# Kernel optimization log

Measured on AMD Instinct MI355X. Metric: run time of the kernel, lower is better.

Reference implementation:

```python
import jax, jax.numpy as jnp
import numpy as np

GAMMA = 0.7


def setup_inputs() -> dict:
    key = jax.random.key(0)
    k1, k2, k3 = jax.random.split(key, 3)
    K, N, M = 8, 2_000_000, 50_000
    states_x = jax.random.normal(k1, (K, N, 3), dtype=jnp.float32)
    x_target = jax.random.normal(k2, (N, 3), dtype=jnp.float32)
    molecule_id = jnp.sort(jax.random.randint(k3, (N,), 0, M, dtype=jnp.int64))
    return {
        "states_x": states_x,
        "x_target": x_target,
        "molecule_id": molecule_id,
        "num_molecules": M,
    }


def reference(states_x, x_target, molecule_id, num_molecules):
    # states_x: (K, N, 3) = refinement states 1..K (state 0 is already dropped)
    # x_target: (N, 3); molecule_id: (N,) segment ids
    K = states_x.shape[0]
    dtype = x_target.dtype
    # exponential weights gamma^(K-1-k), normalized
    w = jnp.power(jnp.asarray(GAMMA, dtype), (K - 1) - jnp.arange(K, dtype=dtype))
    w = w / w.sum()
    # per-atom squared distance per state: (K, N)
    sq = ((states_x - x_target[None]) ** 2).sum(axis=-1)
    # segment-reduce over molecules: sums (M, K), counts (M,)
    sums = jax.ops.segment_sum(sq.T, molecule_id, num_segments=num_molecules)
    counts = jax.ops.segment_sum(
        jnp.ones((molecule_id.shape[0],), dtype=dtype), molecule_id,
        num_segments=num_molecules)
    valid = counts > 0  # pt.unique only iterates over ids that appear
    means = sums / jnp.maximum(counts, 1)[:, None]  # (M, K) per-molecule mean sq dist
    per_state = (means * valid[:, None].astype(dtype)).sum(axis=0) / valid.sum().astype(dtype)
    return (w * per_state).sum()
```

## Files before the change

kernel.cpp:

```cpp
#include <hip/hip_runtime.h>

#define GAMMA 0.7f
static constexpr int K = 8;
static constexpr int P = 1024;


__global__ void __launch_bounds__(256)
main_fused(const float* __restrict__ sx,
           const float* __restrict__ xt,
           const int* __restrict__ mol,
           float* __restrict__ partials,
           int* __restrict__ bcounts,
           int N) {
    const int tid = threadIdx.x;
    const int b0  = blockIdx.x * P;
    const int n0  = b0 + tid * 4;

    __shared__ int ids[P + 2];
    int* w = ids + 1;

    int myid[4];
    if (n0 + 3 < N) {
        int4 v = *reinterpret_cast<const int4*>(mol + n0);
        myid[0] = v.x; myid[1] = v.y; myid[2] = v.z; myid[3] = v.w;
    } else {
#pragma unroll
        for (int j = 0; j < 4; ++j) {
            int n = n0 + j;
            myid[j] = (n < N) ? mol[n] : 0x7fffffff;
        }
    }
#pragma unroll
    for (int j = 0; j < 4; ++j) w[tid * 4 + j] = myid[j];
    if (tid == 0)   ids[0]     = (b0 == 0) ? -1 : mol[b0 - 1];
    if (tid == 255) ids[P + 1] = (b0 + P >= N) ? 0x7fffffff : mol[b0 + P];
    __syncthreads();

    float inv[4];
    int nb = 0;
#pragma unroll
    for (int j = 0; j < 4; ++j) {
        const int p  = tid * 4 + j;
        const int id = myid[j];
        const bool valid = (b0 + p < N);
        const int prevv = (j > 0) ? myid[j - 1] : ids[p];
        if (valid && prevv != id) ++nb;
        if (!valid) { inv[j] = 0.0f; continue; }
        if (j > 0 && myid[j - 1] == id) { inv[j] = inv[j - 1]; continue; }

        int lo = 0, hi = p;
        while (lo < hi) { int m = (lo + hi) >> 1; if (w[m] < id) lo = m + 1; else hi = m; }
        const int s = lo;
        lo = p + 1; hi = P;
        while (lo < hi) { int m = (lo + hi) >> 1; if (w[m] <= id) lo = m + 1; else hi = m; }
        const int e = lo;

        int gstart = b0 + s;
        if (s == 0 && ids[0] == id) {
            lo = 0; hi = b0;
            while (lo < hi) { int m = (lo + hi) >> 1; if (mol[m] < id) lo = m + 1; else hi = m; }
            gstart = lo;
        }
        int gend = b0 + e;
        if (e == P && ids[P + 1] == id) {
            lo = b0 + P; hi = N;
            while (lo < hi) { int m = (lo + hi) >> 1; if (mol[m] <= id) lo = m + 1; else hi = m; }
            gend = lo;
        }
        inv[j] = 1.0f / (float)(gend - gstart);
    }

    float acc[K];
#pragma unroll
    for (int k = 0; k < K; ++k) acc[k] = 0.0f;

    if (n0 + 3 < N) {
        const float4* tp = reinterpret_cast<const float4*>(xt + (size_t)n0 * 3);
        float4 t0 = tp[0], t1 = tp[1], t2 = tp[2];
        float tg[12] = {t0.x, t0.y, t0.z, t0.w, t1.x, t1.y,
                        t1.z, t1.w, t2.x, t2.y, t2.z, t2.w};
#pragma unroll
        for (int k = 0; k < K; ++k) {
            const float4* sp = reinterpret_cast<const float4*>(
                sx + (size_t)k * N * 3 + (size_t)n0 * 3);
            float4 s0 = sp[0], s1 = sp[1], s2 = sp[2];
            float sv[12] = {s0.x, s0.y, s0.z, s0.w, s1.x, s1.y,
                            s1.z, s1.w, s2.x, s2.y, s2.z, s2.w};
#pragma unroll
            for (int j = 0; j < 4; ++j) {
                float dx = sv[3 * j + 0] - tg[3 * j + 0];
                float dy = sv[3 * j + 1] - tg[3 * j + 1];
                float dz = sv[3 * j + 2] - tg[3 * j + 2];
                acc[k] += (dx * dx + dy * dy + dz * dz) * inv[j];
            }
        }
    } else if (n0 < N) {
        for (int n = n0; n < N; ++n) {
            const int j = n - n0;
            float tx = xt[(size_t)n * 3 + 0];
            float ty = xt[(size_t)n * 3 + 1];
            float tz = xt[(size_t)n * 3 + 2];
#pragma unroll
            for (int k = 0; k < K; ++k) {
                const float* s = sx + (size_t)k * N * 3 + (size_t)n * 3;
                float dx = s[0] - tx, dy = s[1] - ty, dz = s[2] - tz;
                acc[k] += (dx * dx + dy * dy + dz * dz) * inv[j];
            }
        }
    }

#pragma unroll
    for (int k = 0; k < K; ++k)
#pragma unroll
        for (int off = 32; off > 0; off >>= 1)
            acc[k] += __shfl_down(acc[k], off, 64);
#pragma unroll
    for (int off = 32; off > 0; off >>= 1) nb += __shfl_down(nb, off, 64);

    __shared__ float lds[4][K];
    __shared__ int   bl[4];
    const int wave = tid >> 6, lane = tid & 63;
    if (lane == 0) {
        bl[wave] = nb;
#pragma unroll
        for (int k = 0; k < K; ++k) lds[wave][k] = acc[k];
    }
    __syncthreads();
    if (tid < K) {
        int k = tid;
        partials[(size_t)blockIdx.x * K + k] =
            lds[0][k] + lds[1][k] + lds[2][k] + lds[3][k];
    }
    if (tid == 0)
        bcounts[blockIdx.x] = bl[0] + bl[1] + bl[2] + bl[3];
}

__global__ void __launch_bounds__(256)
final_kernel(const float* __restrict__ partials,
             const int* __restrict__ bcounts, int nblocks,
             float* __restrict__ out) {
    const int t = threadIdx.x;

    int vc = 0;
    for (int i = t; i < nblocks; i += 256) vc += bcounts[i];
#pragma unroll
    for (int off = 32; off > 0; off >>= 1) vc += __shfl_down(vc, off, 64);

    float acc[K];
#pragma unroll
    for (int k = 0; k < K; ++k) acc[k] = 0.0f;
    for (int i = t; i < nblocks; i += 256) {
#pragma unroll
        for (int k = 0; k < K; ++k) acc[k] += partials[(size_t)i * K + k];
    }
#pragma unroll
    for (int k = 0; k < K; ++k)
#pragma unroll
        for (int off = 32; off > 0; off >>= 1)
            acc[k] += __shfl_down(acc[k], off, 64);

    __shared__ int vlds[4];
    __shared__ float plds[4][K];
    const int wave = t >> 6, lane = t & 63;
    if (lane == 0) {
        vlds[wave] = vc;
#pragma unroll
        for (int k = 0; k < K; ++k) plds[wave][k] = acc[k];
    }
    __syncthreads();

    if (t == 0) {
        int V = vlds[0] + vlds[1] + vlds[2] + vlds[3];
        float w[K], wsum = 0.0f, g = 1.0f;
        for (int j = 0; j < K; ++j) {
            w[K - 1 - j] = g;
            wsum += g;
            g *= GAMMA;
        }
        float invV = (V > 0) ? 1.0f / (float)V : 0.0f;
        float res = 0.0f;
#pragma unroll
        for (int k = 0; k < K; ++k) {
            float ps = (plds[0][k] + plds[1][k] + plds[2][k] + plds[3][k]) * invV;
            res += (w[k] / wsum) * ps;
        }
        out[0] = res;
    }
}

extern "C" void kernel_launch(void* const* d_in, const int* in_sizes, int n_in,
                              void* d_out, int out_size, void* d_ws, size_t ws_size,
                              hipStream_t stream) {
    const float* states_x = (const float*)d_in[0];
    const float* x_target = (const float*)d_in[1];
    const int*   mol      = (const int*)d_in[2];

    const int N = in_sizes[2];
    const int nblocks = (N + P - 1) / P;

    char* ws = (char*)d_ws;
    size_t boff = (((size_t)nblocks * K * 4) + 255) & ~(size_t)255;

    float* partials = (float*)ws;
    int*   bcounts  = (int*)(ws + boff);

    main_fused<<<nblocks, 256, 0, stream>>>(states_x, x_target, mol,
                                            partials, bcounts, N);
    final_kernel<<<1, 256, 0, stream>>>(partials, bcounts, nblocks,
                                        (float*)d_out);
}
```

Baseline: 61.16 us.

## Double per-block atoms, interleave LDS binary searches, use galloping boundary search

After: 83.24 us. 1.36x slower.

```diff
diff --git a/kernel.cpp b/kernel.cpp
--- a/kernel.cpp
+++ b/kernel.cpp
@@ -2,7 +2,7 @@
 
 #define GAMMA 0.7f
 static constexpr int K = 8;
-static constexpr int P = 1024;
+static constexpr int P = 2048;
 
 
 __global__ void __launch_bounds__(256)
@@ -14,33 +14,35 @@
            int N) {
     const int tid = threadIdx.x;
     const int b0  = blockIdx.x * P;
-    const int n0  = b0 + tid * 4;
+    const int n0  = b0 + tid * 8;
 
     __shared__ int ids[P + 2];
     int* w = ids + 1;
 
-    int myid[4];
-    if (n0 + 3 < N) {
-        int4 v = *reinterpret_cast<const int4*>(mol + n0);
-        myid[0] = v.x; myid[1] = v.y; myid[2] = v.z; myid[3] = v.w;
+    int myid[8];
+    if (n0 + 7 < N) {
+        int4 v0 = *reinterpret_cast<const int4*>(mol + n0);
+        int4 v1 = *reinterpret_cast<const int4*>(mol + n0 + 4);
+        myid[0] = v0.x; myid[1] = v0.y; myid[2] = v0.z; myid[3] = v0.w;
+        myid[4] = v1.x; myid[5] = v1.y; myid[6] = v1.z; myid[7] = v1.w;
     } else {
 #pragma unroll
-        for (int j = 0; j < 4; ++j) {
+        for (int j = 0; j < 8; ++j) {
             int n = n0 + j;
             myid[j] = (n < N) ? mol[n] : 0x7fffffff;
         }
     }
 #pragma unroll
-    for (int j = 0; j < 4; ++j) w[tid * 4 + j] = myid[j];
+    for (int j = 0; j < 8; ++j) w[tid * 8 + j] = myid[j];
     if (tid == 0)   ids[0]     = (b0 == 0) ? -1 : mol[b0 - 1];
     if (tid == 255) ids[P + 1] = (b0 + P >= N) ? 0x7fffffff : mol[b0 + P];
     __syncthreads();
 
-    float inv[4];
+    float inv[8];
     int nb = 0;
 #pragma unroll
-    for (int j = 0; j < 4; ++j) {
-        const int p  = tid * 4 + j;
+    for (int j = 0; j < 8; ++j) {
+        const int p  = tid * 8 + j;
         const int id = myid[j];
         const bool valid = (b0 + p < N);
         const int prevv = (j > 0) ? myid[j - 1] : ids[p];
@@ -48,23 +50,40 @@
         if (!valid) { inv[j] = 0.0f; continue; }
         if (j > 0 && myid[j - 1] == id) { inv[j] = inv[j - 1]; continue; }
 
-        int lo = 0, hi = p;
-        while (lo < hi) { int m = (lo + hi) >> 1; if (w[m] < id) lo = m + 1; else hi = m; }
-        const int s = lo;
-        lo = p + 1; hi = P;
-        while (lo < hi) { int m = (lo + hi) >> 1; if (w[m] <= id) lo = m + 1; else hi = m; }
-        const int e = lo;
+        int slo = 0, shi = p, elo = p + 1, ehi = P;
+        while (slo < shi || elo < ehi) {
+            if (slo < shi) {
+                int m = (slo + shi) >> 1;
+                if (w[m] < id) slo = m + 1; else shi = m;
+            }
+            if (elo < ehi) {
+                int m = (elo + ehi) >> 1;
+                if (w[m] <= id) elo = m + 1; else ehi = m;
+            }
+        }
+        const int s = slo, e = elo;
 
         int gstart = b0 + s;
         if (s == 0 && ids[0] == id) {
-            lo = 0; hi = b0;
-            while (lo < hi) { int m = (lo + hi) >> 1; if (mol[m] < id) lo = m + 1; else hi = m; }
+            int hi = b0 - 1, step = 1, lo = hi - 1;
+            while (lo >= 0 && mol[lo] == id) { hi = lo; step <<= 1; lo = hi - step; }
+            ++lo;
+            while (lo < hi) {
+                int m = (lo + hi) >> 1;
+                if (mol[m] < id) lo = m + 1; else hi = m;
+            }
             gstart = lo;
         }
         int gend = b0 + e;
         if (e == P && ids[P + 1] == id) {
-            lo = b0 + P; hi = N;
-            while (lo < hi) { int m = (lo + hi) >> 1; if (mol[m] <= id) lo = m + 1; else hi = m; }
+            int lo = b0 + P, step = 1, probe = lo + step;
+            while (probe < N && mol[probe] == id) { lo = probe; step <<= 1; probe = lo + step; }
+            int hi = (probe < N) ? probe : N;
+            ++lo;
+            while (lo < hi) {
+                int m = (lo + hi) >> 1;
+                if (mol[m] <= id) lo = m + 1; else hi = m;
+            }
             gend = lo;
         }
         inv[j] = 1.0f / (float)(gend - gstart);
@@ -74,20 +93,28 @@
 #pragma unroll
     for (int k = 0; k < K; ++k) acc[k] = 0.0f;
 
-    if (n0 + 3 < N) {
+    if (n0 + 7 < N) {
         const float4* tp = reinterpret_cast<const float4*>(xt + (size_t)n0 * 3);
-        float4 t0 = tp[0], t1 = tp[1], t2 = tp[2];
-        float tg[12] = {t0.x, t0.y, t0.z, t0.w, t1.x, t1.y,
-                        t1.z, t1.w, t2.x, t2.y, t2.z, t2.w};
+        float tg[24];
+#pragma unroll
+        for (int q = 0; q < 6; ++q) {
+            float4 tv = tp[q];
+            tg[q * 4 + 0] = tv.x; tg[q * 4 + 1] = tv.y;
+            tg[q * 4 + 2] = tv.z; tg[q * 4 + 3] = tv.w;
+        }
 #pragma unroll
         for (int k = 0; k < K; ++k) {
             const float4* sp = reinterpret_cast<const float4*>(
                 sx + (size_t)k * N * 3 + (size_t)n0 * 3);
-            float4 s0 = sp[0], s1 = sp[1], s2 = sp[2];
-            float sv[12] = {s0.x, s0.y, s0.z, s0.w, s1.x, s1.y,
-                            s1.z, s1.w, s2.x, s2.y, s2.z, s2.w};
-#pragma unroll
-            for (int j = 0; j < 4; ++j) {
+            float sv[24];
+#pragma unroll
+            for (int q = 0; q < 6; ++q) {
+                float4 s4 = sp[q];
+                sv[q * 4 + 0] = s4.x; sv[q * 4 + 1] = s4.y;
+                sv[q * 4 + 2] = s4.z; sv[q * 4 + 3] = s4.w;
+            }
+#pragma unroll
+            for (int j = 0; j < 8; ++j) {
                 float dx = sv[3 * j + 0] - tg[3 * j + 0];
                 float dy = sv[3 * j + 1] - tg[3 * j + 1];
                 float dz = sv[3 * j + 2] - tg[3 * j + 2];
```
